# Performance work log

Hardware: AMD Instinct MI355X
Metric: run time of the kernel (lower is better)

## Reference

```python
import jax, jax.numpy as jnp
import numpy as np

B, T = 64, 1024
VOCAB, EMBED, HIDDEN = 55, 64, 128


def setup_inputs() -> dict:
    key = jax.random.key(0)
    ks = jax.random.split(key, 15)
    stdv = 1.0 / np.sqrt(HIDDEN)
    u = lambda k, s: jax.random.uniform(k, s, jnp.float32, -stdv, stdv)
    return {
        "x": jax.random.randint(ks[0], (B, T), 0, VOCAB),
        "emb": jax.random.normal(ks[1], (VOCAB, EMBED), jnp.float32),
        "w_ih0": u(ks[2], (HIDDEN, EMBED)),
        "b_ih0": u(ks[3], (HIDDEN,)),
        "w_hh0": u(ks[4], (HIDDEN, HIDDEN)),
        "b_hh0": u(ks[5], (HIDDEN,)),
        "w_ih1": u(ks[6], (HIDDEN, HIDDEN)),
        "b_ih1": u(ks[7], (HIDDEN,)),
        "w_hh1": u(ks[8], (HIDDEN, HIDDEN)),
        "b_hh1": u(ks[9], (HIDDEN,)),
        "attn_w": u(ks[10], (HIDDEN, HIDDEN)),
        "attn_b": u(ks[11], (HIDDEN,)),
        "fc_w": u(ks[12], (VOCAB, 2 * HIDDEN)),
        "fc_b": u(ks[13], (VOCAB,)),
    }


def reference(x, emb, w_ih0, b_ih0, w_hh0, b_hh0, w_ih1, b_ih1, w_hh1, b_hh1,
              attn_w, attn_b, fc_w, fc_b):
    Bx, Tx = x.shape
    H = w_hh0.shape[0]
    e = emb[x]  # [B, T, E]

    def step(carry, x_t):  # x_t: [B, E]
        h0, h1 = carry
        h0 = jnp.tanh(x_t @ w_ih0.T + b_ih0 + h0 @ w_hh0.T + b_hh0)
        h1 = jnp.tanh(h0 @ w_ih1.T + b_ih1 + h1 @ w_hh1.T + b_hh1)
        return (h0, h1), h1

    init = (jnp.zeros((Bx, H), e.dtype), jnp.zeros((Bx, H), e.dtype))
    _, outs = jax.lax.scan(step, init, jnp.swapaxes(e, 0, 1))  # [T, B, H]
    outs = jnp.swapaxes(outs, 0, 1)  # [B, T, H]

    Q = outs @ attn_w.T + attn_b  # [B, T, H]
    scores = jnp.einsum('bth,bsh->bts', Q, outs) / jnp.sqrt(jnp.asarray(H, e.dtype))
    causal = jnp.tril(jnp.ones((Tx, Tx), bool))  # [T, T]
    scores = jnp.where(causal[None], scores, jnp.asarray(-jnp.inf, scores.dtype))
    attn = jax.nn.softmax(scores, axis=-1)
    context = jnp.einsum('bts,bsh->bth', attn, outs)  # [B, T, H]

    combined = jnp.concatenate([outs, context], axis=-1)  # [B, T, 2H]
    logits = combined @ fc_w.T + fc_b  # [B, T, vocab]
    return logits
```

## Files before the change

### kernel.cpp

```cpp
#include <hip/hip_runtime.h>
#include <hip/hip_bf16.h>
#include <cstdint>
#include <cstddef>


typedef __attribute__((ext_vector_type(8))) short short8;
typedef __attribute__((ext_vector_type(4))) float f32x4;

__device__ __forceinline__ float bf2f(unsigned short u) {
    union { unsigned int i; float f; } c; c.i = ((unsigned int)u) << 16; return c.f;
}
__device__ __forceinline__ unsigned short f2bf(float f) {
    union { float f; unsigned int i; } c; c.f = f;
    unsigned int u = c.i;
    u += 0x7fffu + ((u >> 16) & 1u);
    return (unsigned short)(u >> 16);
}
__device__ __forceinline__ unsigned int pk_bf16(float lo, float hi) {
    union { __hip_bfloat162 h2; unsigned int u; } c;
    c.h2 = __float22bfloat162_rn(make_float2(lo, hi));
    return c.u;
}
__device__ __forceinline__ float fast_tanh(float x) {
    float e = __expf(2.0f * x);
    return 1.0f - 2.0f * __builtin_amdgcn_rcpf(e + 1.0f);
}
__device__ __forceinline__ void bar_lds() {
    asm volatile("s_waitcnt lgkmcnt(0)\n\ts_barrier" ::: "memory");
}
__device__ __forceinline__ short8 ld_a_bf16(const float* p) {
    const float4* q = (const float4*)p;
    float4 f0 = q[0], f1 = q[1];
    short8 r;
    r[0]=(short)f2bf(f0.x); r[1]=(short)f2bf(f0.y);
    r[2]=(short)f2bf(f0.z); r[3]=(short)f2bf(f0.w);
    r[4]=(short)f2bf(f1.x); r[5]=(short)f2bf(f1.y);
    r[6]=(short)f2bf(f1.z); r[7]=(short)f2bf(f1.w);
    return r;
}
__device__ __forceinline__ void gload_lds16(const unsigned short* g,
                                            unsigned short* l) {
    __builtin_amdgcn_global_load_lds(
        (const __attribute__((address_space(1))) unsigned int*)g,
        (__attribute__((address_space(3))) unsigned int*)l, 16, 0, 0);
}

__global__ __launch_bounds__(256)
void k_prep(const float* __restrict__ attn_w, const float* __restrict__ fc_w,
            unsigned short* __restrict__ attn_wb,
            unsigned short* __restrict__ fc_hib,
            unsigned short* __restrict__ fc_lob)
{
    const int i = blockIdx.x * 256 + threadIdx.x;
    if (i < 16384) attn_wb[i] = f2bf(attn_w[i]);
    if (i < 14080) {
        float wv = fc_w[i];
        unsigned short h = f2bf(wv);
        fc_hib[i] = h;
        fc_lob[i] = f2bf(wv - bf2f(h));
    }
}

__global__ __launch_bounds__(128)
void k_we(const float* __restrict__ emb, const float* __restrict__ w_ih0,
          const float* __restrict__ b_ih0, const float* __restrict__ b_hh0,
          float* __restrict__ WE)
{
    __shared__ float ev[64];
    const int i = threadIdx.x;
    const int v = blockIdx.x;
    if (i < 64) ev[i] = emb[v * 64 + i];
    __syncthreads();
    float s = b_ih0[i] + b_hh0[i];
    const float* wr = w_ih0 + i * 64;
#pragma unroll
    for (int k = 0; k < 64; ++k) s += wr[k] * ev[k];
    WE[v * 128 + i] = s;
}

__global__ __launch_bounds__(256)
void k_weg(const int* __restrict__ x, const float* __restrict__ WE,
           float* __restrict__ WEg)
{
    __shared__ int xv[32];
    const int tid = threadIdx.x;
    const int b   = blockIdx.y;
    const int t0  = blockIdx.x * 32;
    if (tid < 32) xv[tid] = x[b * 1024 + t0 + tid];
    __syncthreads();
#pragma unroll
    for (int it = 0; it < 4; ++it) {
        int tt = it * 8 + (tid >> 5);
        int c4 = tid & 31;
        float4 v = ((const float4*)(WE + xv[tt] * 128))[c4];
        ((float4*)(WEg + ((size_t)b * 1024 + t0 + tt) * 128))[c4] = v;
    }
}

#define A_STEP(T, P, E0, E1)                                                   \
  {                                                                            \
    const unsigned short* h0p = &h0buf[P][n][quad * 8];                        \
    short8 bh[4];                                                              \
    _Pragma("unroll")                                                          \
    for (int ks = 0; ks < 4; ++ks)                                             \
      bh[ks] = *(const short8*)(h0p + ks * 32);                                \
    f32x4 c0 = (f32x4){E0.x, E0.y, E0.z, E0.w};                                \
    f32x4 c1 = (f32x4){E1.x, E1.y, E1.z, E1.w};                                \
    {                                                                          \
      const size_t tp = (size_t)(((T) + 3 < 1024) ? (T) + 3 : 1023) * 128;     \
      E0 = *(const float4*)(WEg + wegB0 + tp);                                 \
      E1 = *(const float4*)(WEg + wegB1 + tp);                                 \
    }                                                                          \
    _Pragma("unroll")                                                          \
    for (int ks = 0; ks < 4; ++ks) {                                           \
      c0 = __builtin_amdgcn_mfma_f32_16x16x32_bf16(a0[0][ks], bh[ks], c0, 0, 0, 0); \
      c1 = __builtin_amdgcn_mfma_f32_16x16x32_bf16(a0[1][ks], bh[ks], c1, 0, 0, 0); \
    }                                                                          \
    *(uint2*)&h0buf[(P) ^ 1][n][r0] = make_uint2(                              \
        pk_bf16(fast_tanh(c0[0]), fast_tanh(c0[1])),                           \
        pk_bf16(fast_tanh(c0[2]), fast_tanh(c0[3])));                          \
    *(uint2*)&h0buf[(P) ^ 1][n][r1] = make_uint2(                              \
        pk_bf16(fast_tanh(c1[0]), fast_tanh(c1[1])),                           \
        pk_bf16(fast_tanh(c1[2]), fast_tanh(c1[3])));                          \
    bar_lds();                                                                 \
  }

#define B_STEP(T, P)                                                           \
  {                                                                            \
    const unsigned short* h0p = &h0buf[P][n][quad * 8];                        \
    const unsigned short* h1p = &h1buf[P][n][quad * 8];                        \
    short8 bh0[4], bh1[4];                                                     \
    _Pragma("unroll")                                                          \
    for (int ks = 0; ks < 4; ++ks) {                                           \
      bh0[ks] = *(const short8*)(h0p + ks * 32);                               \
      bh1[ks] = *(const short8*)(h1p + ks * 32);                               \
    }                                                                          \
    f32x4 c0 = b1i[0], c1 = b1i[1];                                            \
    f32x4 d0 = (f32x4){0.f, 0.f, 0.f, 0.f};                                    \
    f32x4 d1 = (f32x4){0.f, 0.f, 0.f, 0.f};                                    \
    _Pragma("unroll")                                                          \
    for (int ks = 0; ks < 4; ++ks) {                                           \
      c0 = __builtin_amdgcn_mfma_f32_16x16x32_bf16(a1[0][ks], bh0[ks], c0, 0, 0, 0); \
      c1 = __builtin_amdgcn_mfma_f32_16x16x32_bf16(a1[1][ks], bh0[ks], c1, 0, 0, 0); \
      d0 = __builtin_amdgcn_mfma_f32_16x16x32_bf16(a2[0][ks], bh1[ks], d0, 0, 0, 0); \
      d1 = __builtin_amdgcn_mfma_f32_16x16x32_bf16(a2[1][ks], bh1[ks], d1, 0, 0, 0); \
    }                                                                          \
    uint2 o0 = make_uint2(                                                     \
        pk_bf16(fast_tanh(c0[0] + d0[0]), fast_tanh(c0[1] + d0[1])),           \
        pk_bf16(fast_tanh(c0[2] + d0[2]), fast_tanh(c0[3] + d0[3])));          \
    uint2 o1 = make_uint2(                                                     \
        pk_bf16(fast_tanh(c1[0] + d1[0]), fast_tanh(c1[1] + d1[1])),           \
        pk_bf16(fast_tanh(c1[2] + d1[2]), fast_tanh(c1[3] + d1[3])));          \
    *(uint2*)&h1buf[(P) ^ 1][n][r0] = o0;                                      \
    *(uint2*)&h1buf[(P) ^ 1][n][r1] = o1;                                      \
    *(uint2*)(outp0 + (size_t)(T) * 128) = o0;                                 \
    *(uint2*)(outp1 + (size_t)(T) * 128) = o1;                                 \
    bar_lds();                                                                 \
  }

__global__ __launch_bounds__(512, 1)
void k_scan7(const float* __restrict__ WEg,
             const float* __restrict__ w_hh0,
             const float* __restrict__ w_ih1, const float* __restrict__ b_ih1,
             const float* __restrict__ w_hh1, const float* __restrict__ b_hh1,
             unsigned short* __restrict__ outs_bf)
{
    const int tid   = threadIdx.x;
    const int w     = tid >> 6;
    const int lane  = tid & 63;
    const int quad  = lane >> 4;
    const int n     = lane & 15;
    const int bbase = blockIdx.x * 16;

    __shared__ __align__(16) unsigned short h0buf[2][16][136];
    __shared__ __align__(16) unsigned short h1buf[2][16][136];

    if (w < 4) {
        const int r0 = w * 32 + quad * 4;
        const int r1 = r0 + 16;
        short8 a0[2][4];
#pragma unroll
        for (int r = 0; r < 2; ++r) {
            const size_t mrow = (size_t)(w * 32 + r * 16 + n) * 128;
#pragma unroll
            for (int ks = 0; ks < 4; ++ks)
                a0[r][ks] = ld_a_bf16(w_hh0 + mrow + ks * 32 + quad * 8);
        }
        const size_t wegB0 = (size_t)(bbase + n) * 131072 + r0;
        const size_t wegB1 = wegB0 + 16;
        {
            float4 p0 = *(const float4*)(WEg + wegB0);
            float4 p1 = *(const float4*)(WEg + wegB1);
            *(uint2*)&h0buf[0][n][r0] = make_uint2(
                pk_bf16(fast_tanh(p0.x), fast_tanh(p0.y)),
                pk_bf16(fast_tanh(p0.z), fast_tanh(p0.w)));
            *(uint2*)&h0buf[0][n][r1] = make_uint2(
                pk_bf16(fast_tanh(p1.x), fast_tanh(p1.y)),
                pk_bf16(fast_tanh(p1.z), fast_tanh(p1.w)));
        }
        float4 eA0 = *(const float4*)(WEg + wegB0 + 128);
        float4 eA1 = *(const float4*)(WEg + wegB1 + 128);
        float4 eB0 = *(const float4*)(WEg + wegB0 + 256);
        float4 eB1 = *(const float4*)(WEg + wegB1 + 256);
        __syncthreads();

        for (int t = 0; t < 1022; t += 2) {
            A_STEP(t,     0, eA0, eA1);
            A_STEP(t + 1, 1, eB0, eB1);
        }
        A_STEP(1022, 0, eA0, eA1);
        bar_lds();
    } else {
        const int w2 = w - 4;
        const int r0 = w2 * 32 + quad * 4;
        const int r1 = r0 + 16;
        short8 a1[2][4], a2[2][4];
#pragma unroll
        for (int r = 0; r < 2; ++r) {
            const size_t mrow = (size_t)(w2 * 32 + r * 16 + n) * 128;
#pragma unroll
            for (int ks = 0; ks < 4; ++ks) {
                a1[r][ks] = ld_a_bf16(w_ih1 + mrow + ks * 32 + quad * 8);
                a2[r][ks] = ld_a_bf16(w_hh1 + mrow + ks * 32 + quad * 8);
            }
        }
        f32x4 b1i[2];
#pragma unroll
        for (int r = 0; r < 2; ++r)
#pragma unroll
            for (int j = 0; j < 4; ++j) {
                int row = w2 * 32 + r * 16 + quad * 4 + j;
                b1i[r][j] = b_ih1[row] + b_hh1[row];
            }
        *(uint2*)&h1buf[0][n][r0] = make_uint2(0u, 0u);
        *(uint2*)&h1buf[0][n][r1] = make_uint2(0u, 0u);
        unsigned short* outp0 = outs_bf + (size_t)(bbase + n) * 131072 + r0;
        unsigned short* outp1 = outp0 + 16;
        __syncthreads();

        for (int t = 0; t < 1022; t += 2) {
            B_STEP(t,     0);
            B_STEP(t + 1, 1);
        }
        B_STEP(1022, 0);
        B_STEP(1023, 1);
    }
}

__global__ __launch_bounds__(256)
void k_transpose(const unsigned short* __restrict__ outs_bf,
                 unsigned short* __restrict__ outsT)
{
    __shared__ unsigned short lt[128][130];
    const int tid = threadIdx.x;
    const int t0  = blockIdx.x * 128;
    const int b   = blockIdx.y;
    const unsigned int* src =
        (const unsigned int*)(outs_bf + ((size_t)b * 1024 + t0) * 128);
    for (int idx = tid; idx < 8192; idx += 256) {
        int tr = idx >> 6, h2 = idx & 63;
        unsigned int v = src[tr * 64 + h2];
        lt[tr][h2 * 2]     = (unsigned short)(v & 0xffffu);
        lt[tr][h2 * 2 + 1] = (unsigned short)(v >> 16);
    }
    __syncthreads();
    unsigned int* dst = (unsigned int*)(outsT + (size_t)b * 128 * 1024);
    for (int idx = tid; idx < 8192; idx += 256) {
        int h = idx >> 6, t2 = idx & 63;
        unsigned int v = (unsigned int)lt[t2 * 2][h] |
                         ((unsigned int)lt[t2 * 2 + 1][h] << 16);
        dst[h * 512 + (t0 >> 1) + t2] = v;
    }
}

__global__ __launch_bounds__(512, 1)
void k_attnfc(const unsigned short* __restrict__ outs_bf,
              const unsigned short* __restrict__ outsT,
              const unsigned short* __restrict__ attn_wb,
              const float* __restrict__ attn_b,
              const unsigned short* __restrict__ fc_hib,
              const unsigned short* __restrict__ fc_lob,
              const float* __restrict__ fc_b,
              float* __restrict__ out)
{
    __shared__ __align__(16) unsigned char smem[51200];
    unsigned short* lK = (unsigned short*)smem;
    unsigned short* lV = (unsigned short*)(smem + 16384);
    unsigned short* lP = (unsigned short*)(smem + 32768);

    const int tid  = threadIdx.x;
    const int w    = tid >> 6;
    const int lane = tid & 63;
    const int quad = lane >> 4;
    const int n    = lane & 15;
    const int qt   = blockIdx.x;
    const int b    = blockIdx.y;
    unsigned short* lPw = lP + w * 1152;
    unsigned short* lQw = ((unsigned short*)smem) + w * 2048;
    const float cscale = 0.08838834764831845f;

    const unsigned short* outsB = outs_bf + (size_t)b * 131072;
    const int qrow = qt * 128 + w * 16 + n;

    short8 bo[4];
#pragma unroll
    for (int ks = 0; ks < 4; ++ks)
        bo[ks] = *(const short8*)(outsB + (size_t)qrow * 128 + ks * 32 + quad * 8);
#pragma unroll
    for (int mt = 0; mt < 8; ++mt) {
        short8 aw[4];
#pragma unroll
        for (int ks = 0; ks < 4; ++ks)
            aw[ks] = *(const short8*)(attn_wb + (size_t)(mt * 16 + n) * 128 +
                                      ks * 32 + quad * 8);
        f32x4 cq;
#pragma unroll
        for (int r = 0; r < 4; ++r) cq[r] = attn_b[mt * 16 + quad * 4 + r];
#pragma unroll
        for (int ks = 0; ks < 4; ++ks)
            cq = __builtin_amdgcn_mfma_f32_16x16x32_bf16(aw[ks], bo[ks], cq, 0,0,0);
        *(uint2*)&lQw[n * 128 + mt * 16 + quad * 4] =
            make_uint2(pk_bf16(cq[0], cq[1]), pk_bf16(cq[2], cq[3]));
    }
    short8 qf[4];
#pragma unroll
    for (int ks = 0; ks < 4; ++ks)
        qf[ks] = *(const short8*)&lQw[n * 128 + ks * 32 + quad * 8];

    f32x4 accO[8];
#pragma unroll
    for (int dt = 0; dt < 8; ++dt) accO[dt] = (f32x4){0.f, 0.f, 0.f, 0.f};
    float mx = -1e30f, lsum = 0.f;

    const int ntiles = 2 * qt + 2;
    for (int kt = 0; kt < ntiles; ++kt) {
        __syncthreads();
        {
            int c = tid;
            int row = c >> 4, g = c & 15;
            gload_lds16(outsB + (size_t)(kt * 64 + row) * 128 +
                        ((g ^ (row & 15)) << 3), lK + c * 8);
            c = tid + 512; row = c >> 4; g = c & 15;
            gload_lds16(outsB + (size_t)(kt * 64 + row) * 128 +
                        ((g ^ (row & 15)) << 3), lK + c * 8);
            int c2 = tid;
            int d = c2 >> 3, t8 = c2 & 7;
            gload_lds16(outsT + ((size_t)b * 128 + d) * 1024 + kt * 64 +
                        ((t8 ^ (d & 7)) << 3), lV + c2 * 8);
            c2 = tid + 512; d = c2 >> 3; t8 = c2 & 7;
            gload_lds16(outsT + ((size_t)b * 128 + d) * 1024 + kt * 64 +
                        ((t8 ^ (d & 7)) << 3), lV + c2 * 8);
        }
        __syncthreads();
        f32x4 accS[4];
#pragma unroll
        for (int mt = 0; mt < 4; ++mt) {
            short8 af[4];
#pragma unroll
            for (int ks = 0; ks < 4; ++ks) {
                int r = mt * 16 + n;
                af[ks] = *(const short8*)&lK[r * 128 + (((ks * 4 + quad) ^ (r & 15)) << 3)];
            }
            f32x4 s = (f32x4){0.f, 0.f, 0.f, 0.f};
#pragma unroll
            for (int ks = 0; ks < 4; ++ks)
                s = __builtin_amdgcn_mfma_f32_16x16x32_bf16(af[ks], qf[ks], s, 0,0,0);
            accS[mt] = s;
        }
        if (kt >= 2 * qt) {
            const int ql = w * 16 + n;
#pragma unroll
            for (int mt = 0; mt < 4; ++mt)
#pragma unroll
                for (int jv = 0; jv < 4; ++jv)
                    if (kt * 64 + mt * 16 + quad * 4 + jv > qt * 128 + ql)
                        accS[mt][jv] = -1e30f;
        }
        float tmax = accS[0][0];
#pragma unroll
        for (int mt = 0; mt < 4; ++mt)
#pragma unroll
            for (int jv = 0; jv < 4; ++jv) tmax = fmaxf(tmax, accS[mt][jv]);
        tmax = fmaxf(tmax, __shfl_xor(tmax, 16));
        tmax = fmaxf(tmax, __shfl_xor(tmax, 32));
        float nm = fmaxf(mx, tmax);
        float alpha = __expf((mx - nm) * cscale);
        float ss = 0.f;
#pragma unroll
        for (int mt = 0; mt < 4; ++mt)
#pragma unroll
            for (int jv = 0; jv < 4; ++jv) {
                float p = __expf((accS[mt][jv] - nm) * cscale);
                accS[mt][jv] = p;
                ss += p;
            }
        ss += __shfl_xor(ss, 16);
        ss += __shfl_xor(ss, 32);
        lsum = lsum * alpha + ss;
        mx = nm;
#pragma unroll
        for (int mt = 0; mt < 4; ++mt)
            *(uint2*)&lPw[n * 72 + mt * 16 + quad * 4] = make_uint2(
                pk_bf16(accS[mt][0], accS[mt][1]),
                pk_bf16(accS[mt][2], accS[mt][3]));
#pragma unroll
        for (int dt = 0; dt < 8; ++dt)
#pragma unroll
            for (int jv = 0; jv < 4; ++jv) accO[dt][jv] *= alpha;
        short8 pf[2];
#pragma unroll
        for (int ks = 0; ks < 2; ++ks)
            pf[ks] = *(const short8*)&lPw[n * 72 + ks * 32 + quad * 8];
#pragma unroll
        for (int dt = 0; dt < 8; ++dt) {
            short8 vf[2];
#pragma unroll
            for (int ks = 0; ks < 2; ++ks) {
                int d = dt * 16 + n;
                vf[ks] = *(const short8*)&lV[d * 64 + (((ks * 4 + quad) ^ (d & 7)) << 3)];
            }
#pragma unroll
            for (int ks = 0; ks < 2; ++ks)
                accO[dt] = __builtin_amdgcn_mfma_f32_16x16x32_bf16(vf[ks], pf[ks], accO[dt], 0,0,0);
        }
    }
    __syncthreads();
    {
        float inv = __builtin_amdgcn_rcpf(lsum);
#pragma unroll
        for (int dt = 0; dt < 8; ++dt)
            *(uint2*)&lQw[n * 128 + dt * 16 + quad * 4] = make_uint2(
                pk_bf16(accO[dt][0] * inv, accO[dt][1] * inv),
                pk_bf16(accO[dt][2] * inv, accO[dt][3] * inv));
    }
    short8 bC[4];
#pragma unroll
    for (int ks = 0; ks < 4; ++ks)
        bC[ks] = *(const short8*)&lQw[n * 128 + ks * 32 + quad * 8];
#pragma unroll
    for (int mt = 0; mt < 4; ++mt) {
        const int vrow = mt * 16 + n;
        f32x4 acc;
#pragma unroll
        for (int r = 0; r < 4; ++r) {
            int vv = mt * 16 + quad * 4 + r;
            acc[r] = (vv < 55) ? fc_b[vv] : 0.f;
        }
#pragma unroll
        for (int c = 0; c < 8; ++c) {
            short8 hi, lo;
            if (vrow < 55) {
                hi = *(const short8*)(fc_hib + (size_t)vrow * 256 + c * 32 + quad * 8);
                lo = *(const short8*)(fc_lob + (size_t)vrow * 256 + c * 32 + quad * 8);
            } else {
#pragma unroll
                for (int i = 0; i < 8; ++i) { hi[i] = 0; lo[i] = 0; }
            }
            short8 bb = (c < 4) ? bo[c] : bC[c - 4];
            acc = __builtin_amdgcn_mfma_f32_16x16x32_bf16(hi, bb, acc, 0,0,0);
            acc = __builtin_amdgcn_mfma_f32_16x16x32_bf16(lo, bb, acc, 0,0,0);
        }
#pragma unroll
        for (int r = 0; r < 4; ++r) {
            int vv = mt * 16 + quad * 4 + r;
            if (vv < 55)
                out[((size_t)b * 1024 + qrow) * 55 + vv] = acc[r];
        }
    }
}

extern "C" void kernel_launch(void* const* d_in, const int* in_sizes, int n_in,
                              void* d_out, int out_size, void* d_ws, size_t ws_size,
                              hipStream_t stream)
{
    const int*   x      = (const int*)d_in[0];
    const float* emb    = (const float*)d_in[1];
    const float* w_ih0  = (const float*)d_in[2];
    const float* b_ih0  = (const float*)d_in[3];
    const float* w_hh0  = (const float*)d_in[4];
    const float* b_hh0  = (const float*)d_in[5];
    const float* w_ih1  = (const float*)d_in[6];
    const float* b_ih1  = (const float*)d_in[7];
    const float* w_hh1  = (const float*)d_in[8];
    const float* b_hh1  = (const float*)d_in[9];
    const float* attn_w = (const float*)d_in[10];
    const float* attn_b = (const float*)d_in[11];
    const float* fc_w   = (const float*)d_in[12];
    const float* fc_b   = (const float*)d_in[13];
    float* out = (float*)d_out;

    char* ws = (char*)d_ws;
    unsigned short* outs_bf = (unsigned short*)(ws);
    unsigned short* outsT   = (unsigned short*)(ws + ((size_t)16 << 20));
    float*          WEp     = (float*)         (ws + ((size_t)32 << 20));
    unsigned short* attn_wb = (unsigned short*)(ws + ((size_t)32 << 20) + (64 << 10));
    unsigned short* fc_hib  = (unsigned short*)(ws + ((size_t)32 << 20) + (128 << 10));
    unsigned short* fc_lob  = (unsigned short*)(ws + ((size_t)32 << 20) + (192 << 10));
    float*          WEg     = (float*)         (ws + ((size_t)33 << 20));

    k_prep<<<dim3(64), dim3(256), 0, stream>>>(attn_w, fc_w, attn_wb, fc_hib, fc_lob);
    k_we<<<dim3(55), dim3(128), 0, stream>>>(emb, w_ih0, b_ih0, b_hh0, WEp);
    k_weg<<<dim3(32, 64), dim3(256), 0, stream>>>(x, WEp, WEg);
    k_scan7<<<dim3(4), dim3(512), 0, stream>>>(
        WEg, w_hh0, w_ih1, b_ih1, w_hh1, b_hh1, outs_bf);
    k_transpose<<<dim3(8, 64), dim3(256), 0, stream>>>(outs_bf, outsT);
    k_attnfc<<<dim3(8, 64), dim3(512), 0, stream>>>(
        outs_bf, outsT, attn_wb, attn_b, fc_hib, fc_lob, fc_b, out);
}
```

Measured before the change: 744.6 us.

## Read K/V fragments directly from global memory and drop shared-memory staging in attention

```diff
diff --git a/kernel.cpp b/kernel.cpp
--- a/kernel.cpp
+++ b/kernel.cpp
@@ -37,12 +37,6 @@
     r[4]=(short)f2bf(f1.x); r[5]=(short)f2bf(f1.y);
     r[6]=(short)f2bf(f1.z); r[7]=(short)f2bf(f1.w);
     return r;
-}
-__device__ __forceinline__ void gload_lds16(const unsigned short* g,
-                                            unsigned short* l) {
-    __builtin_amdgcn_global_load_lds(
-        (const __attribute__((address_space(1))) unsigned int*)g,
-        (__attribute__((address_space(3))) unsigned int*)l, 16, 0, 0);
 }
 
 __global__ __launch_bounds__(256)
@@ -273,7 +267,7 @@
     }
 }
 
-__global__ __launch_bounds__(512, 1)
+__global__ __launch_bounds__(512, 4)
 void k_attnfc(const unsigned short* __restrict__ outs_bf,
               const unsigned short* __restrict__ outsT,
               const unsigned short* __restrict__ attn_wb,
@@ -283,10 +277,7 @@
               const float* __restrict__ fc_b,
               float* __restrict__ out)
 {
-    __shared__ __align__(16) unsigned char smem[51200];
-    unsigned short* lK = (unsigned short*)smem;
-    unsigned short* lV = (unsigned short*)(smem + 16384);
-    unsigned short* lP = (unsigned short*)(smem + 32768);
+    __shared__ __align__(16) unsigned short lB[8][2176];
 
     const int tid  = threadIdx.x;
     const int w    = tid >> 6;
@@ -295,11 +286,11 @@
     const int n    = lane & 15;
     const int qt   = blockIdx.x;
     const int b    = blockIdx.y;
-    unsigned short* lPw = lP + w * 1152;
-    unsigned short* lQw = ((unsigned short*)smem) + w * 2048;
+    unsigned short* lBw = lB[w];
     const float cscale = 0.08838834764831845f;
 
     const unsigned short* outsB = outs_bf + (size_t)b * 131072;
+    const unsigned short* outsTB = outsT + (size_t)b * 131072;
     const int qrow = qt * 128 + w * 16 + n;
 
     short8 bo[4];
@@ -319,13 +310,13 @@
 #pragma unroll
         for (int ks = 0; ks < 4; ++ks)
             cq = __builtin_amdgcn_mfma_f32_16x16x32_bf16(aw[ks], bo[ks], cq, 0,0,0);
-        *(uint2*)&lQw[n * 128 + mt * 16 + quad * 4] =
+        *(uint2*)&lBw[n * 136 + mt * 16 + quad * 4] =
             make_uint2(pk_bf16(cq[0], cq[1]), pk_bf16(cq[2], cq[3]));
     }
     short8 qf[4];
 #pragma unroll
     for (int ks = 0; ks < 4; ++ks)
-        qf[ks] = *(const short8*)&lQw[n * 128 + ks * 32 + quad * 8];
+        qf[ks] = *(const short8*)&lBw[n * 136 + ks * 32 + quad * 8];
 
     f32x4 accO[8];
 #pragma unroll
@@ -334,33 +325,14 @@
 
     const int ntiles = 2 * qt + 2;
     for (int kt = 0; kt < ntiles; ++kt) {
-        __syncthreads();
-        {
-            int c = tid;
-            int row = c >> 4, g = c & 15;
-            gload_lds16(outsB + (size_t)(kt * 64 + row) * 128 +
-                        ((g ^ (row & 15)) << 3), lK + c * 8);
-            c = tid + 512; row = c >> 4; g = c & 15;
-            gload_lds16(outsB + (size_t)(kt * 64 + row) * 128 +
-                        ((g ^ (row & 15)) << 3), lK + c * 8);
-            int c2 = tid;
-            int d = c2 >> 3, t8 = c2 & 7;
-            gload_lds16(outsT + ((size_t)b * 128 + d) * 1024 + kt * 64 +
-                        ((t8 ^ (d & 7)) << 3), lV + c2 * 8);
-            c2 = tid + 512; d = c2 >> 3; t8 = c2 & 7;
-            gload_lds16(outsT + ((size_t)b * 128 + d) * 1024 + kt * 64 +
-                        ((t8 ^ (d & 7)) << 3), lV + c2 * 8);
-        }
-        __syncthreads();
         f32x4 accS[4];
 #pragma unroll
         for (int mt = 0; mt < 4; ++mt) {
             short8 af[4];
 #pragma unroll
-            for (int ks = 0; ks < 4; ++ks) {
-                int r = mt * 16 + n;
-                af[ks] = *(const short8*)&lK[r * 128 + (((ks * 4 + quad) ^ (r & 15)) << 3)];
-            }
+            for (int ks = 0; ks < 4; ++ks)
+                af[ks] = *(const short8*)(outsB +
+                    (size_t)(kt * 64 + mt * 16 + n) * 128 + ks * 32 + quad * 8);
             f32x4 s = (f32x4){0.f, 0.f, 0.f, 0.f};
 #pragma unroll
             for (int ks = 0; ks < 4; ++ks)
@@ -400,7 +372,7 @@
         mx = nm;
 #pragma unroll
         for (int mt = 0; mt < 4; ++mt)
-            *(uint2*)&lPw[n * 72 + mt * 16 + quad * 4] = make_uint2(
+            *(uint2*)&lBw[n * 136 + mt * 16 + quad * 4] = make_uint2(
                 pk_bf16(accS[mt][0], accS[mt][1]),
                 pk_bf16(accS[mt][2], accS[mt][3]));
 #pragma unroll
@@ -410,33 +382,31 @@
         short8 pf[2];
 #pragma unroll
         for (int ks = 0; ks < 2; ++ks)
-            pf[ks] = *(const short8*)&lPw[n * 72 + ks * 32 + quad * 8];
+            pf[ks] = *(const short8*)&lBw[n * 136 + ks * 32 + quad * 8];
 #pragma unroll
         for (int dt = 0; dt < 8; ++dt) {
             short8 vf[2];
 #pragma unroll
-            for (int ks = 0; ks < 2; ++ks) {
-                int d = dt * 16 + n;
-                vf[ks] = *(const short8*)&lV[d * 64 + (((ks * 4 + quad) ^ (d & 7)) << 3)];
-            }
+            for (int ks = 0; ks < 2; ++ks)
+                vf[ks] = *(const short8*)(outsTB +
+                    (size_t)(dt * 16 + n) * 1024 + kt * 64 + ks * 32 + quad * 8);
 #pragma unroll
             for (int ks = 0; ks < 2; ++ks)
                 accO[dt] = __builtin_amdgcn_mfma_f32_16x16x32_bf16(vf[ks], pf[ks], accO[dt], 0,0,0);
         }
     }
-    __syncthreads();
     {
         float inv = __builtin_amdgcn_rcpf(lsum);
 #pragma unroll
         for (int dt = 0; dt < 8; ++dt)
-            *(uint2*)&lQw[n * 128 + dt * 16 + quad * 4] = make_uint2(
+            *(uint2*)&lBw[n * 136 + dt * 16 + quad * 4] = make_uint2(
                 pk_bf16(accO[dt][0] * inv, accO[dt][1] * inv),
                 pk_bf16(accO[dt][2] * inv, accO[dt][3] * inv));
     }
     short8 bC[4];
 #pragma unroll
     for (int ks = 0; ks < 4; ++ks)
-        bC[ks] = *(const short8*)&lQw[n * 128 + ks * 32 + quad * 8];
+        bC[ks] = *(const short8*)&lBw[n * 136 + ks * 32 + quad * 8];
 #pragma unroll
     for (int mt = 0; mt < 4; ++mt) {
         const int vrow = mt * 16 + n;
```

Result: slower. 905.4 us (+21.6%).
